# Optimization experiments

Hardware: AMD Instinct MI355X
Metric: run time of the kernel (lower is better)

The kernel has to match this reference:

```python
import jax, jax.numpy as jnp
import numpy as np
from jax import lax

CONF_THRES = 0.25
IOU_THRES = 0.45
MAX_WH = 4096.0   # class offset, agnostic=False
MAX_DET = 300
NEG = jnp.float32(-1e30)


def setup_inputs() -> dict:
    key = jax.random.key(0)
    B, N, C = 16, 25200, 85  # 640x640 yolov5, nc=80
    k1, k2, k3, k4 = jax.random.split(key, 4)
    xy = jax.random.uniform(k1, (B, N, 2), jnp.float32, 0.0, 640.0)
    wh = jax.random.uniform(k2, (B, N, 2), jnp.float32, 4.0, 120.0)
    obj = jax.random.uniform(k3, (B, N, 1), jnp.float32)
    cls = jax.random.uniform(k4, (B, N, C - 5), jnp.float32)
    prediction = jnp.concatenate([xy, wh, obj, cls], axis=-1)
    return {"prediction": prediction}


def _xywh2xyxy(b):
    # b: [N,4] (cx,cy,w,h) -> (x1,y1,x2,y2)
    return jnp.concatenate([b[:, :2] - b[:, 2:4] * 0.5,
                            b[:, :2] + b[:, 2:4] * 0.5], axis=1)


def _iou_one_vs_all(box, boxes):
    # box: [4], boxes: [N,4], plain IoU as in torchvision.ops.nms
    x1 = jnp.maximum(box[0], boxes[:, 0])
    y1 = jnp.maximum(box[1], boxes[:, 1])
    x2 = jnp.minimum(box[2], boxes[:, 2])
    y2 = jnp.minimum(box[3], boxes[:, 3])
    inter = jnp.clip(x2 - x1, 0.0) * jnp.clip(y2 - y1, 0.0)
    a1 = (box[2] - box[0]) * (box[3] - box[1])
    a2 = (boxes[:, 2] - boxes[:, 0]) * (boxes[:, 3] - boxes[:, 1])
    return inter / (a1 + a2 - inter)


def _nms_image(p):
    # p: [N, 5+nc] single-image predictions (decoded xywh, obj, class scores)
    obj = p[:, 4]                               # [N]
    cls_scores = p[:, 5:] * obj[:, None]        # x[:,5:] *= x[:,4:5]
    conf = jnp.max(cls_scores, axis=1)          # best-class conf
    j = jnp.argmax(cls_scores, axis=1)          # best class id
    boxes = _xywh2xyxy(p[:, :4])                # [N,4]
    valid = (obj > CONF_THRES) & (conf > CONF_THRES)
    # class-offset boxes for per-class NMS (agnostic=False)
    nms_boxes = boxes + (j.astype(boxes.dtype) * MAX_WH)[:, None]

    s0 = jnp.where(valid, conf, NEG)

    def step(s_live, _):
        i = jnp.argmax(s_live)
        sel = s_live[i]
        keep = sel > 0.0
        iou = _iou_one_vs_all(nms_boxes[i], nms_boxes)
        suppress = keep & (iou > IOU_THRES)
        s_new = jnp.where(suppress, NEG, s_live).at[i].set(NEG)
        return s_new, (i, keep)

    _, (idxs, keeps) = lax.scan(step, s0, None, length=MAX_DET)
    # output rows [x1,y1,x2,y2,conf,cls] — boxes WITHOUT class offset
    rows = jnp.concatenate([boxes[idxs], conf[idxs, None],
                            j[idxs, None].astype(boxes.dtype)], axis=1)
    rows = rows * keeps[:, None].astype(rows.dtype)  # zero padded slots
    return rows, keeps


def reference(prediction):
    # prediction: [B, N, 5+nc] -> ([B, MAX_DET, 6], [B, MAX_DET] keep mask)
    out, keep = jax.vmap(_nms_image)(prediction)
    return out, keep
```

## Files before the change

kernel.cpp:

```cpp
#include <hip/hip_runtime.h>
#include <cstdint>
#include <cfloat>

#define BATCH 16
#define NBOX 25200
#define CH 85
#define NCLS 80
#define CAP 512
#define ACC 48
#define MAXDET 300
#define RPB 128
#define CNTPAD 16

typedef unsigned long long u64;

__device__ __forceinline__ u64 shflx64(u64 v, int m) {
    int lo = __shfl_xor((int)(unsigned)(v & 0xffffffffu), m);
    int hi = __shfl_xor((int)(unsigned)(v >> 32), m);
    return ((u64)(unsigned)hi << 32) | (u64)(unsigned)lo;
}

__global__ __launch_bounds__(256) void pre_kernel(const float* __restrict__ p,
                                                  int* __restrict__ cnt,
                                                  u64* __restrict__ bucketKey) {
#pragma clang fp contract(off)
    __shared__ float s[RPB * CH];
    int tid = threadIdx.x;
    long blockRow = (long)blockIdx.x * RPB;

    const float4* p4 = (const float4*)(p + blockRow * CH);
    float4* s4 = (float4*)s;
    for (int t = tid; t < RPB * CH / 4; t += 256) {
        __builtin_amdgcn_global_load_lds(
            (const __attribute__((address_space(1))) void*)(p4 + t),
            (__attribute__((address_space(3))) void*)(s4 + (t & ~63)),
            16, 0, 0);
    }
    __syncthreads();

    int r = tid >> 1;
    int half = tid & 1;
    const float* row = s + r * CH;
    float obj = row[4];

    float v = -FLT_MAX; int c = 1000;
    int c0 = half * 40;
    for (int k = 0; k < 40; k++) {
        float sc = row[5 + c0 + k] * obj;
        int cc = c0 + k;
        if (sc > v) { v = sc; c = cc; }
    }
    float v2 = __shfl_xor(v, 1);
    int   cz = __shfl_xor(c, 1);
    if (v2 > v || (v2 == v && cz < c)) { v = v2; c = cz; }

    if (half == 0 && obj > 0.25f && v > 0.25f) {
        int wid = (int)blockRow + r;
        int b   = wid / NBOX;
        int idx = wid - b * NBOX;
        u64 key = ((u64)__float_as_uint(v) << 22) | ((u64)(32767 - idx) << 7) | (u64)c;
        int bkt = b * NCLS + c;
        int pos = atomicAdd(&cnt[bkt * CNTPAD], 1);
        if (pos < CAP) bucketKey[(long)bkt * CAP + pos] = key;
    }
}

__global__ __launch_bounds__(256) void nms_kernel(const float* __restrict__ p,
                                                  const int* __restrict__ cnt,
                                                  const u64* __restrict__ bucketKey,
                                                  u64* __restrict__ accKey) {
#pragma clang fp contract(off)
    int lane = threadIdx.x & 63;
    int bkt = (blockIdx.x << 2) | (threadIdx.x >> 6);
    int b = bkt / NCLS, c = bkt - b * NCLS;
    int n = cnt[bkt * CNTPAD]; if (n > CAP) n = CAP;

    u64 key[8];
#pragma unroll
    for (int r = 0; r < 8; r++) {
        int pos = (r << 6) | lane;
        key[r] = (pos < n) ? bucketKey[(long)bkt * CAP + pos] : 0ULL;
    }

    auto CE_lane = [&](int k, int j) {
#pragma unroll
        for (int r = 0; r < 8; r++) {
            u64 part = shflx64(key[r], j);
            int pos = (r << 6) | lane;
            bool keepmax = (((pos & k) == 0) == ((lane & j) == 0));
            u64 mx = (key[r] > part) ? key[r] : part;
            u64 mn = (key[r] > part) ? part : key[r];
            key[r] = keepmax ? mx : mn;
        }
    };

#pragma unroll
    for (int k = 2; k <= 64; k <<= 1)
        for (int j = k >> 1; j > 0; j >>= 1)
            CE_lane(k, j);

#define CE_REG(K, M)                                                   \
    {                                                                  \
        _Pragma("unroll")                                              \
        for (int r = 0; r < 8; r++) if (!(r & (M))) {                  \
            int r2 = r | (M);                                          \
            u64 a = key[r], d = key[r2];                               \
            bool desc = (((r << 6) & (K)) == 0);                       \
            u64 hi = (a > d) ? a : d, lo = (a > d) ? d : a;            \
            key[r]  = desc ? hi : lo;                                  \
            key[r2] = desc ? lo : hi;                                  \
        }                                                              \
    }

    CE_REG(128, 1)
    for (int j = 32; j > 0; j >>= 1) CE_lane(128, j);
    CE_REG(256, 2) CE_REG(256, 1)
    for (int j = 32; j > 0; j >>= 1) CE_lane(256, j);
    CE_REG(512, 4) CE_REG(512, 2) CE_REG(512, 1)
    for (int j = 32; j > 0; j >>= 1) CE_lane(512, j);
#undef CE_REG

    float off = (float)c * 4096.0f;
    float rx1[8], ry1[8], rx2[8], ry2[8], rar[8];
    int live = 0;
#pragma unroll
    for (int r = 0; r < 8; r++) {
        int pos = (r << 6) | lane;
        rx1[r] = 0.f; ry1[r] = 0.f; rx2[r] = 0.f; ry2[r] = 0.f; rar[r] = 0.f;
        if (pos < n) {
            int idx = 32767 - (int)((key[r] >> 7) & 32767);
            const float* q = p + ((long)b * NBOX + idx) * CH;
            float x = q[0], y = q[1], w = q[2], h = q[3];
            float hw = w * 0.5f, hh = h * 0.5f;
            rx1[r] = (x - hw) + off; ry1[r] = (y - hh) + off;
            rx2[r] = (x + hw) + off; ry2[r] = (y + hh) + off;
            rar[r] = (rx2[r] - rx1[r]) * (ry2[r] - ry1[r]);
            live |= 1 << r;
        }
    }

    long obase = (long)bkt * ACC;
    int nacc = 0;
    for (;;) {
        int i = -1;
#pragma unroll
        for (int r = 0; r < 8; r++) {
            u64 mr = __ballot((live >> r) & 1);
            if (i < 0 && mr) i = (r << 6) + (int)__ffsll((long long)mr) - 1;
        }
        if (i < 0) break;
        int ro = i >> 6, owner = i & 63;

        u64 kk; float sX1, sY1, sX2, sY2, sA;
        switch (ro) {
            case 0: kk=key[0]; sX1=rx1[0]; sY1=ry1[0]; sX2=rx2[0]; sY2=ry2[0]; sA=rar[0]; break;
            case 1: kk=key[1]; sX1=rx1[1]; sY1=ry1[1]; sX2=rx2[1]; sY2=ry2[1]; sA=rar[1]; break;
            case 2: kk=key[2]; sX1=rx1[2]; sY1=ry1[2]; sX2=rx2[2]; sY2=ry2[2]; sA=rar[2]; break;
            case 3: kk=key[3]; sX1=rx1[3]; sY1=ry1[3]; sX2=rx2[3]; sY2=ry2[3]; sA=rar[3]; break;
            case 4: kk=key[4]; sX1=rx1[4]; sY1=ry1[4]; sX2=rx2[4]; sY2=ry2[4]; sA=rar[4]; break;
            case 5: kk=key[5]; sX1=rx1[5]; sY1=ry1[5]; sX2=rx2[5]; sY2=ry2[5]; sA=rar[5]; break;
            case 6: kk=key[6]; sX1=rx1[6]; sY1=ry1[6]; sX2=rx2[6]; sY2=ry2[6]; sA=rar[6]; break;
            default:kk=key[7]; sX1=rx1[7]; sY1=ry1[7]; sX2=rx2[7]; sY2=ry2[7]; sA=rar[7]; break;
        }
        if (lane == owner) {
            accKey[obase + nacc] = kk;
            live &= ~(1 << ro);
        }
        nacc++;
        if (nacc == ACC) break;

        float X1 = __shfl(sX1, owner), Y1 = __shfl(sY1, owner);
        float X2 = __shfl(sX2, owner), Y2 = __shfl(sY2, owner);
        float A  = __shfl(sA,  owner);

#pragma unroll
        for (int r = 0; r < 8; r++) {
            if ((live >> r) & 1) {
                float xx1 = fmaxf(X1, rx1[r]);
                float yy1 = fmaxf(Y1, ry1[r]);
                float xx2 = fminf(X2, rx2[r]);
                float yy2 = fminf(Y2, ry2[r]);
                float inter = fmaxf(xx2 - xx1, 0.0f) * fmaxf(yy2 - yy1, 0.0f);
                float uni = (A + rar[r]) - inter;
                if (inter / uni > 0.45f) live &= ~(1 << r);
            }
        }
    }
    for (int t = nacc + lane; t < ACC; t += 64) accKey[obase + t] = 0ULL;
}

__global__ __launch_bounds__(256) void merge_kernel(const float* __restrict__ p,
                                                    const u64* __restrict__ accKey,
                                                    float* __restrict__ outRows,
                                                    float* __restrict__ outKeep) {
#pragma clang fp contract(off)
    __shared__ u64 L[NCLS * ACC];
    int tid = threadIdx.x;
    int b = blockIdx.y;
    const u64* src = accKey + (long)b * NCLS * ACC;
    for (int t = tid; t < NCLS * ACC; t += 256) L[t] = src[t];
    __syncthreads();

    int g = blockIdx.x * 256 + tid;
    u64 key = L[g];
    if (key == 0ULL) return;
    int cOwn = g / ACC;
    int rank = g - cOwn * ACC;

    for (int d = 1; d < NCLS; d++) {
        int c2 = cOwn + d; if (c2 >= NCLS) c2 -= NCLS;
        const u64* Lc = L + c2 * ACC;
        int cn = 0;
#pragma unroll
        for (int s2 = 32; s2; s2 >>= 1) {
            int nc = cn + s2;
            if (nc <= ACC && Lc[nc - 1] > key) cn = nc;
        }
        rank += cn;
        if (rank >= MAXDET) return;
    }

    int cc  = (int)(key & 127);
    int idx = 32767 - (int)((key >> 7) & 32767);
    float conf = __uint_as_float((unsigned)(key >> 22));
    const float* q = p + ((long)b * NBOX + idx) * CH;
    float x = q[0], y = q[1], w = q[2], h = q[3];
    float hw = w * 0.5f, hh = h * 0.5f;
    float* row = outRows + ((long)b * MAXDET + rank) * 6;
    row[0] = x - hw; row[1] = y - hh; row[2] = x + hw; row[3] = y + hh;
    row[4] = conf;   row[5] = (float)cc;
    outKeep[b * MAXDET + rank] = 1.0f;
}

extern "C" void kernel_launch(void* const* d_in, const int* in_sizes, int n_in,
                              void* d_out, int out_size, void* d_ws, size_t ws_size,
                              hipStream_t stream) {
    const float* p = (const float*)d_in[0];
    float* out = (float*)d_out;

    char* ws = (char*)d_ws;
    int* cnt = (int*)ws;
    u64* bucketKey = (u64*)(ws + BATCH * NCLS * CNTPAD * 4);
    u64* accKey    = (u64*)(ws + BATCH * NCLS * CNTPAD * 4
                               + (size_t)BATCH * NCLS * CAP * 8);

    hipMemsetAsync(cnt, 0, BATCH * NCLS * CNTPAD * sizeof(int), stream);
    hipMemsetAsync(out, 0, (size_t)out_size * sizeof(float), stream);
    pre_kernel<<<(BATCH * NBOX) / RPB, 256, 0, stream>>>(p, cnt, bucketKey);
    nms_kernel<<<BATCH * NCLS / 4, 256, 0, stream>>>(p, cnt, bucketKey, accKey);
    dim3 gM(NCLS * ACC / 256, BATCH);
    merge_kernel<<<gM, 256, 0, stream>>>(p, accKey, out, out + (size_t)BATCH * MAXDET * 6);
}
```

Baseline: 306.4 us.

## Specialize NMS sort width, quarter-row argmax, and linear-scan merge ranking

Result: no change. 311.5 us (+1.7%).

```diff
diff --git a/kernel.cpp b/kernel.cpp
--- a/kernel.cpp
+++ b/kernel.cpp
@@ -9,7 +9,7 @@
 #define CAP 512
 #define ACC 48
 #define MAXDET 300
-#define RPB 128
+#define RPB 64
 #define CNTPAD 16
 
 typedef unsigned long long u64;
@@ -38,23 +38,26 @@
     }
     __syncthreads();
 
-    int r = tid >> 1;
-    int half = tid & 1;
+    int r = tid >> 2;
+    int q = tid & 3;
     const float* row = s + r * CH;
     float obj = row[4];
 
     float v = -FLT_MAX; int c = 1000;
-    int c0 = half * 40;
-    for (int k = 0; k < 40; k++) {
+    int c0 = q * 20;
+    for (int k = 0; k < 20; k++) {
         float sc = row[5 + c0 + k] * obj;
         int cc = c0 + k;
         if (sc > v) { v = sc; c = cc; }
     }
-    float v2 = __shfl_xor(v, 1);
-    int   cz = __shfl_xor(c, 1);
-    if (v2 > v || (v2 == v && cz < c)) { v = v2; c = cz; }
-
-    if (half == 0 && obj > 0.25f && v > 0.25f) {
+#pragma unroll
+    for (int m = 1; m <= 2; m <<= 1) {
+        float v2 = __shfl_xor(v, m);
+        int   cz = __shfl_xor(c, m);
+        if (v2 > v || (v2 == v && cz < c)) { v = v2; c = cz; }
+    }
+
+    if (q == 0 && obj > 0.25f && v > 0.25f) {
         int wid = (int)blockRow + r;
         int b   = wid / NBOX;
         int idx = wid - b * NBOX;
@@ -65,66 +68,70 @@
     }
 }
 
-__global__ __launch_bounds__(256) void nms_kernel(const float* __restrict__ p,
-                                                  const int* __restrict__ cnt,
-                                                  const u64* __restrict__ bucketKey,
-                                                  u64* __restrict__ accKey) {
+template<int R>
+__device__ __forceinline__ void wave_sort(u64 (&key)[R], int lane) {
+#pragma unroll
+    for (int k = 2; k <= 64; k <<= 1)
+#pragma unroll
+        for (int j = k >> 1; j > 0; j >>= 1) {
+#pragma unroll
+            for (int r = 0; r < R; r++) {
+                u64 part = shflx64(key[r], j);
+                int pos = (r << 6) | lane;
+                bool keepmax = (((pos & k) == 0) == ((lane & j) == 0));
+                u64 mx = key[r] > part ? key[r] : part;
+                u64 mn = key[r] > part ? part : key[r];
+                key[r] = keepmax ? mx : mn;
+            }
+        }
+#pragma unroll
+    for (int K = 128; K <= R * 64; K <<= 1) {
+#pragma unroll
+        for (int m = K >> 7; m >= 1; m >>= 1) {
+#pragma unroll
+            for (int r = 0; r < R; r++) if (!(r & m)) {
+                int r2 = r | m;
+                u64 a = key[r], d = key[r2];
+                bool desc = (((r << 6) & K) == 0);
+                u64 hi = a > d ? a : d, lo = a > d ? d : a;
+                key[r]  = desc ? hi : lo;
+                key[r2] = desc ? lo : hi;
+            }
+        }
+#pragma unroll
+        for (int j = 32; j > 0; j >>= 1) {
+#pragma unroll
+            for (int r = 0; r < R; r++) {
+                u64 part = shflx64(key[r], j);
+                int pos = (r << 6) | lane;
+                bool keepmax = (((pos & K) == 0) == ((lane & j) == 0));
+                u64 mx = key[r] > part ? key[r] : part;
+                u64 mn = key[r] > part ? part : key[r];
+                key[r] = keepmax ? mx : mn;
+            }
+        }
+    }
+}
+
+template<int R>
+__device__ __forceinline__ void nms_core(int lane, int b, int c, int n, long kbase,
+                                         const float* __restrict__ p,
+                                         const u64* __restrict__ bucketKey,
+                                         u64* __restrict__ accKey, long obase) {
 #pragma clang fp contract(off)
-    int lane = threadIdx.x & 63;
-    int bkt = (blockIdx.x << 2) | (threadIdx.x >> 6);
-    int b = bkt / NCLS, c = bkt - b * NCLS;
-    int n = cnt[bkt * CNTPAD]; if (n > CAP) n = CAP;
-
-    u64 key[8];
-#pragma unroll
-    for (int r = 0; r < 8; r++) {
+    u64 key[R];
+#pragma unroll
+    for (int r = 0; r < R; r++) {
         int pos = (r << 6) | lane;
-        key[r] = (pos < n) ? bucketKey[(long)bkt * CAP + pos] : 0ULL;
-    }
-
-    auto CE_lane = [&](int k, int j) {
-#pragma unroll
-        for (int r = 0; r < 8; r++) {
-            u64 part = shflx64(key[r], j);
-            int pos = (r << 6) | lane;
-            bool keepmax = (((pos & k) == 0) == ((lane & j) == 0));
-            u64 mx = (key[r] > part) ? key[r] : part;
-            u64 mn = (key[r] > part) ? part : key[r];
-            key[r] = keepmax ? mx : mn;
-        }
-    };
-
-#pragma unroll
-    for (int k = 2; k <= 64; k <<= 1)
-        for (int j = k >> 1; j > 0; j >>= 1)
-            CE_lane(k, j);
-
-#define CE_REG(K, M)                                                   \
-    {                                                                  \
-        _Pragma("unroll")                                              \
-        for (int r = 0; r < 8; r++) if (!(r & (M))) {                  \
-            int r2 = r | (M);                                          \
-            u64 a = key[r], d = key[r2];                               \
-            bool desc = (((r << 6) & (K)) == 0);                       \
-            u64 hi = (a > d) ? a : d, lo = (a > d) ? d : a;            \
-            key[r]  = desc ? hi : lo;                                  \
-            key[r2] = desc ? lo : hi;                                  \
-        }                                                              \
-    }
-
-    CE_REG(128, 1)
-    for (int j = 32; j > 0; j >>= 1) CE_lane(128, j);
-    CE_REG(256, 2) CE_REG(256, 1)
-    for (int j = 32; j > 0; j >>= 1) CE_lane(256, j);
-    CE_REG(512, 4) CE_REG(512, 2) CE_REG(512, 1)
-    for (int j = 32; j > 0; j >>= 1) CE_lane(512, j);
-#undef CE_REG
+        key[r] = (pos < n) ? bucketKey[kbase + pos] : 0ULL;
+    }
+    wave_sort<R>(key, lane);
 
     float off = (float)c * 4096.0f;
-    float rx1[8], ry1[8], rx2[8], ry2[8], rar[8];
+    float rx1[R], ry1[R], rx2[R], ry2[R], rar[R];
     int live = 0;
 #pragma unroll
-    for (int r = 0; r < 8; r++) {
+    for (int r = 0; r < R; r++) {
         int pos = (r << 6) | lane;
         rx1[r] = 0.f; ry1[r] = 0.f; rx2[r] = 0.f; ry2[r] = 0.f; rar[r] = 0.f;
         if (pos < n) {
@@ -139,28 +146,21 @@
         }
     }
 
-    long obase = (long)bkt * ACC;
     int nacc = 0;
     for (;;) {
         int i = -1;
 #pragma unroll
-        for (int r = 0; r < 8; r++) {
+        for (int r = 0; r < R; r++) {
             u64 mr = __ballot((live >> r) & 1);
             if (i < 0 && mr) i = (r << 6) + (int)__ffsll((long long)mr) - 1;
         }
         if (i < 0) break;
         int ro = i >> 6, owner = i & 63;
 
-        u64 kk; float sX1, sY1, sX2, sY2, sA;
-        switch (ro) {
-            case 0: kk=key[0]; sX1=rx1[0]; sY1=ry1[0]; sX2=rx2[0]; sY2=ry2[0]; sA=rar[0]; break;
-            case 1: kk=key[1]; sX1=rx1[1]; sY1=ry1[1]; sX2=rx2[1]; sY2=ry2[1]; sA=rar[1]; break;
-            case 2: kk=key[2]; sX1=rx1[2]; sY1=ry1[2]; sX2=rx2[2]; sY2=ry2[2]; sA=rar[2]; break;
-            case 3: kk=key[3]; sX1=rx1[3]; sY1=ry1[3]; sX2=rx2[3]; sY2=ry2[3]; sA=rar[3]; break;
-            case 4: kk=key[4]; sX1=rx1[4]; sY1=ry1[4]; sX2=rx2[4]; sY2=ry2[4]; sA=rar[4]; break;
-            case 5: kk=key[5]; sX1=rx1[5]; sY1=ry1[5]; sX2=rx2[5]; sY2=ry2[5]; sA=rar[5]; break;
-            case 6: kk=key[6]; sX1=rx1[6]; sY1=ry1[6]; sX2=rx2[6]; sY2=ry2[6]; sA=rar[6]; break;
-            default:kk=key[7]; sX1=rx1[7]; sY1=ry1[7]; sX2=rx2[7]; sY2=ry2[7]; sA=rar[7]; break;
+        u64 kk = 0; float sX1 = 0, sY1 = 0, sX2 = 0, sY2 = 0, sA = 0;
+#pragma unroll
+        for (int r = 0; r < R; r++) if (r == ro) {
+            kk = key[r]; sX1 = rx1[r]; sY1 = ry1[r]; sX2 = rx2[r]; sY2 = ry2[r]; sA = rar[r];
         }
         if (lane == owner) {
             accKey[obase + nacc] = kk;
@@ -174,19 +174,31 @@
         float A  = __shfl(sA,  owner);
 
 #pragma unroll
-        for (int r = 0; r < 8; r++) {
-            if ((live >> r) & 1) {
-                float xx1 = fmaxf(X1, rx1[r]);
-                float yy1 = fmaxf(Y1, ry1[r]);
-                float xx2 = fminf(X2, rx2[r]);
-                float yy2 = fminf(Y2, ry2[r]);
-                float inter = fmaxf(xx2 - xx1, 0.0f) * fmaxf(yy2 - yy1, 0.0f);
-                float uni = (A + rar[r]) - inter;
-                if (inter / uni > 0.45f) live &= ~(1 << r);
-            }
+        for (int r = 0; r < R; r++) if ((live >> r) & 1) {
+            float xx1 = fmaxf(X1, rx1[r]);
+            float yy1 = fmaxf(Y1, ry1[r]);
+            float xx2 = fminf(X2, rx2[r]);
+            float yy2 = fminf(Y2, ry2[r]);
+            float inter = fmaxf(xx2 - xx1, 0.0f) * fmaxf(yy2 - yy1, 0.0f);
+            float uni = (A + rar[r]) - inter;
+            if (inter / uni > 0.45f) live &= ~(1 << r);
         }
     }
     for (int t = nacc + lane; t < ACC; t += 64) accKey[obase + t] = 0ULL;
+}
+
+__global__ __launch_bounds__(256) void nms_kernel(const float* __restrict__ p,
+                                                  const int* __restrict__ cnt,
+                                                  const u64* __restrict__ bucketKey,
+                                                  u64* __restrict__ accKey) {
+    int lane = threadIdx.x & 63;
+    int bkt = (blockIdx.x << 2) | (threadIdx.x >> 6);
+    int b = bkt / NCLS, c = bkt - b * NCLS;
+    int n = cnt[bkt * CNTPAD]; if (n > CAP) n = CAP;
+    long kbase = (long)bkt * CAP;
+    long obase = (long)bkt * ACC;
+    if (n <= 256) nms_core<4>(lane, b, c, n, kbase, p, bucketKey, accKey, obase);
+    else          nms_core<8>(lane, b, c, n, kbase, p, bucketKey, accKey, obase);
 }
 
 __global__ __launch_bounds__(256) void merge_kernel(const float* __restrict__ p,
@@ -195,30 +207,30 @@
                                                     float* __restrict__ outKeep) {
 #pragma clang fp contract(off)
     __shared__ u64 L[NCLS * ACC];
-    int tid = threadIdx.x;
-    int b = blockIdx.y;
+    int tid = threadIdx.x, b = blockIdx.y;
     const u64* src = accKey + (long)b * NCLS * ACC;
     for (int t = tid; t < NCLS * ACC; t += 256) L[t] = src[t];
     __syncthreads();
 
     int g = blockIdx.x * 256 + tid;
     u64 key = L[g];
-    if (key == 0ULL) return;
-    int cOwn = g / ACC;
-    int rank = g - cOwn * ACC;
-
-    for (int d = 1; d < NCLS; d++) {
-        int c2 = cOwn + d; if (c2 >= NCLS) c2 -= NCLS;
-        const u64* Lc = L + c2 * ACC;
+    int rank = 0;
+    const ulonglong2* L2 = (const ulonglong2*)L;
+    for (int c2 = 0; c2 < NCLS; c2++) {
+        const ulonglong2* Lc = L2 + c2 * (ACC / 2);
         int cn = 0;
 #pragma unroll
-        for (int s2 = 32; s2; s2 >>= 1) {
-            int nc = cn + s2;
-            if (nc <= ACC && Lc[nc - 1] > key) cn = nc;
+        for (int t2 = 0; t2 < ACC / 2; t2++) {
+            ulonglong2 e = Lc[t2];
+            cn += (e.x > key) ? 1 : 0;
+            cn += (e.y > key) ? 1 : 0;
         }
         rank += cn;
-        if (rank >= MAXDET) return;
-    }
+        if ((c2 & 7) == 7) {
+            if (__ballot(key != 0ULL && rank < MAXDET) == 0ULL) return;
+        }
+    }
+    if (key == 0ULL || rank >= MAXDET) return;
 
     int cc  = (int)(key & 127);
     int idx = 32767 - (int)((key >> 7) & 32767);
```
